# Kernel tuning notes

Hardware: AMD Instinct MI355X
Metric: run time of the kernel (lower is better)

The kernel has to match this reference:

```python
import jax, jax.numpy as jnp
import numpy as np

N = 100000      # total nodes across the batch of graphs
E = 1600000     # total edges (avg degree 16)
D = 128         # dim_drug (== num_feature here)
L = 3           # layer_drug
G = 2048        # number of graphs in the batch
BN_EPS = 1e-5


def setup_inputs() -> dict:
    key = jax.random.key(0)
    ks = jax.random.split(key, 10)
    x = jax.random.normal(ks[0], (N, D), dtype=jnp.float32)
    edge_index = jax.random.randint(ks[1], (2, E), 0, N, dtype=jnp.int64)
    batch = jnp.sort(jax.random.randint(ks[2], (N,), 0, G, dtype=jnp.int64))
    s = 0.05
    W1 = jax.random.normal(ks[3], (L, D, D), dtype=jnp.float32) * s
    b1 = jax.random.normal(ks[4], (L, D), dtype=jnp.float32) * s
    W2 = jax.random.normal(ks[5], (L, D, D), dtype=jnp.float32) * s
    b2 = jax.random.normal(ks[6], (L, D), dtype=jnp.float32) * s
    gamma = jnp.ones((L, D), dtype=jnp.float32)
    beta = jnp.zeros((L, D), dtype=jnp.float32)
    return {"x": x, "edge_index": edge_index, "batch": batch,
            "W1": W1, "b1": b1, "W2": W2, "b2": b2,
            "gamma": gamma, "beta": beta}


def reference(x, edge_index, batch, W1, b1, W2, b2, gamma, beta):
    src, dst = edge_index[0], edge_index[1]
    h = x
    layer_outs = []
    for i in range(L):
        # GINConv, eps=0: MLP( (1+eps)*h + sum_{j->i} h_j )
        agg = jax.ops.segment_sum(h[src], dst, num_segments=N)  # [N, D]
        m = agg + h
        m = jax.nn.relu(m @ W1[i] + b1[i]) @ W2[i] + b2[i]       # 2-layer MLP
        m = jax.nn.relu(m)                                        # F.relu after conv
        # BatchNorm1d (training mode: batch stats over node dim, biased var)
        mean = jnp.mean(m, axis=0)
        var = jnp.mean((m - mean) ** 2, axis=0)
        h = gamma[i] * (m - mean) * jax.lax.rsqrt(var + BN_EPS) + beta[i]
        layer_outs.append(h)
    node_rep = jnp.concatenate(layer_outs, axis=1)  # JK 'cat' -> [N, L*D]
    return jax.ops.segment_max(node_rep, batch, num_segments=G)  # [G, L*D]
```

## Files before the change

kernel.cpp:

```cpp
#include <hip/hip_runtime.h>
#include <stdint.h>

#define NN 100000
#define NE 1600000
#define DD 128
#define NL 3
#define NG 2048
#define BN_EPS 1e-5f
#define CAP 56
#define NXCD 8
#define WIN 12500

typedef short s16x8 __attribute__((ext_vector_type(8)));
typedef float f32x4 __attribute__((ext_vector_type(4)));

__device__ __forceinline__ unsigned short f2bfu(float f) {
    union { float f; unsigned int i; } x; x.f = f;
    unsigned int r = x.i + 0x7fffu + ((x.i >> 16) & 1u);
    return (unsigned short)(r >> 16);
}
__device__ __forceinline__ float bfu2f(unsigned short u) {
    union { unsigned int i; float f; } x; x.i = ((unsigned int)u) << 16; return x.f;
}
__device__ __forceinline__ float uplo(unsigned int u) {
    union { unsigned int i; float f; } x; x.i = u << 16; return x.f;
}
__device__ __forceinline__ float uphi(unsigned int u) {
    union { unsigned int i; float f; } x; x.i = u & 0xffff0000u; return x.f;
}
__device__ __forceinline__ void add8(float* a, uint4 v) {
    a[0] += uplo(v.x); a[1] += uphi(v.x);
    a[2] += uplo(v.y); a[3] += uphi(v.y);
    a[4] += uplo(v.z); a[5] += uphi(v.z);
    a[6] += uplo(v.w); a[7] += uphi(v.w);
}
__device__ __forceinline__ unsigned int pack2(float a, float b) {
    return (unsigned int)f2bfu(a) | ((unsigned int)f2bfu(b) << 16);
}

__global__ __launch_bounds__(256) void k_cvt(
    const float* __restrict__ x, unsigned short* __restrict__ hb)
{
    int i = (blockIdx.x * 256 + threadIdx.x) * 4;
    if (i >= NN * DD) return;
    float4 v = *(const float4*)(x + i);
    ushort4 o;
    o.x = f2bfu(v.x); o.y = f2bfu(v.y); o.z = f2bfu(v.z); o.w = f2bfu(v.w);
    *(ushort4*)(hb + i) = o;
}

__global__ __launch_bounds__(256) void k_wtrans(
    const float* __restrict__ W1, const float* __restrict__ W2,
    unsigned short* __restrict__ Wt)
{
    int idx = blockIdx.x * 256 + threadIdx.x;
    if (idx >= 6 * DD * DD) return;
    int mat = idx >> 14;
    int r = idx & 16383;
    int n = r >> 7, k = r & 127;
    const float* src = (mat < 3) ? (W1 + mat * DD * DD) : (W2 + (mat - 3) * DD * DD);
    Wt[idx] = f2bfu(src[k * DD + n]);
}

__global__ __launch_bounds__(256) void k_bounds(
    const int* __restrict__ batch, int* __restrict__ start)
{
    int n = blockIdx.x * 256 + threadIdx.x;
    if (n >= NN) return;
    int bn = batch[n];
    bn = bn < 0 ? 0 : (bn > NG - 1 ? NG - 1 : bn);
    int bp;
    if (n == 0) bp = -1;
    else {
        bp = batch[n - 1];
        bp = bp < 0 ? 0 : (bp > NG - 1 ? NG - 1 : bp);
    }
    for (int g = bp + 1; g <= bn; ++g) start[g] = n;
    if (n == NN - 1) {
        for (int g = bn + 1; g <= NG; ++g) start[g] = NN;
    }
}

__global__ __launch_bounds__(256) void k_fill2(
    const int* __restrict__ ei, int* __restrict__ cnt, int* __restrict__ csr)
{
    const int xcd = blockIdx.x & 7;
    const int slice = blockIdx.x >> 3;
    const int wlo = xcd * WIN, whi = wlo + WIN;
    int e0 = (slice * 256 + threadIdx.x) * 4;
    if (e0 >= NE) return;
    const int* dp = ei + NE + e0;
    int dd[4];
    dd[0] = __builtin_nontemporal_load(dp + 0);
    dd[1] = __builtin_nontemporal_load(dp + 1);
    dd[2] = __builtin_nontemporal_load(dp + 2);
    dd[3] = __builtin_nontemporal_load(dp + 3);
    bool any = false;
    #pragma unroll
    for (int i = 0; i < 4; ++i)
        any |= (dd[i] >= wlo && dd[i] < whi);
    if (!any) return;
    const int* sp = ei + e0;
    int ss[4];
    ss[0] = __builtin_nontemporal_load(sp + 0);
    ss[1] = __builtin_nontemporal_load(sp + 1);
    ss[2] = __builtin_nontemporal_load(sp + 2);
    ss[3] = __builtin_nontemporal_load(sp + 3);
    #pragma unroll
    for (int i = 0; i < 4; ++i) {
        int src = ss[i], dst = dd[i];
        if (dst < wlo || dst >= whi) continue;
        if ((unsigned)src >= NN) continue;
        int pos = atomicAdd(&cnt[dst], 1);
        if (pos < CAP) csr[dst * CAP + pos] = src;
    }
}

__global__ __launch_bounds__(256) void k_agg(
    const unsigned short* __restrict__ hb, const int* __restrict__ cnt,
    const int* __restrict__ csr, unsigned short* __restrict__ aggf)
{
    const int node = blockIdx.x * 16 + (threadIdx.x >> 4);
    const int lane = threadIdx.x & 15;
    if (node >= NN) return;
    int deg = cnt[node];
    deg = deg > CAP ? CAP : deg;
    const int* bkt = csr + node * CAP;
    const unsigned short* base = hb + lane * 8;
    float acc[8];
    {
        uint4 v = *(const uint4*)(base + (long long)node * DD);
        acc[0] = uplo(v.x); acc[1] = uphi(v.x);
        acc[2] = uplo(v.y); acc[3] = uphi(v.y);
        acc[4] = uplo(v.z); acc[5] = uphi(v.z);
        acc[6] = uplo(v.w); acc[7] = uphi(v.w);
    }
    int e = 0;
    for (; e + 8 <= deg; e += 8) {
        int4 i0 = *(const int4*)(bkt + e);
        int4 i1 = *(const int4*)(bkt + e + 4);
        uint4 v0 = *(const uint4*)(base + (long long)i0.x * DD);
        uint4 v1 = *(const uint4*)(base + (long long)i0.y * DD);
        uint4 v2 = *(const uint4*)(base + (long long)i0.z * DD);
        uint4 v3 = *(const uint4*)(base + (long long)i0.w * DD);
        uint4 v4 = *(const uint4*)(base + (long long)i1.x * DD);
        uint4 v5 = *(const uint4*)(base + (long long)i1.y * DD);
        uint4 v6 = *(const uint4*)(base + (long long)i1.z * DD);
        uint4 v7 = *(const uint4*)(base + (long long)i1.w * DD);
        add8(acc, v0); add8(acc, v1); add8(acc, v2); add8(acc, v3);
        add8(acc, v4); add8(acc, v5); add8(acc, v6); add8(acc, v7);
    }
    for (; e + 4 <= deg; e += 4) {
        int4 i0 = *(const int4*)(bkt + e);
        uint4 v0 = *(const uint4*)(base + (long long)i0.x * DD);
        uint4 v1 = *(const uint4*)(base + (long long)i0.y * DD);
        uint4 v2 = *(const uint4*)(base + (long long)i0.z * DD);
        uint4 v3 = *(const uint4*)(base + (long long)i0.w * DD);
        add8(acc, v0); add8(acc, v1); add8(acc, v2); add8(acc, v3);
    }
    for (; e < deg; ++e) {
        uint4 v = *(const uint4*)(base + (long long)bkt[e] * DD);
        add8(acc, v);
    }
    uint4 o;
    o.x = pack2(acc[0], acc[1]);
    o.y = pack2(acc[2], acc[3]);
    o.z = pack2(acc[4], acc[5]);
    o.w = pack2(acc[6], acc[7]);
    *(uint4*)(aggf + (long long)node * DD + lane * 8) = o;
}

__global__ __launch_bounds__(256, 2) void k_mlp(
    const unsigned short* __restrict__ aggf, unsigned short* __restrict__ hb,
    const unsigned short* __restrict__ W1t, const float* __restrict__ b1,
    const unsigned short* __restrict__ W2t, const float* __restrict__ b2,
    float* __restrict__ stats)
{
    __shared__ unsigned short lA[128 * 136];
    __shared__ unsigned short lW[128 * 136];
    __shared__ float sSum[4][128];
    __shared__ float sSq[4][128];
    const int tid = threadIdx.x;
    const int row0 = blockIdx.x * 128;

    #pragma unroll
    for (int it = 0; it < 8; ++it) {
        int eidx = (it * 256 + tid) * 8;
        int r = eidx >> 7, c = eidx & 127;
        *(uint4*)(&lW[r * 136 + c]) = *(const uint4*)(W1t + eidx);
    }
    {
        int col8 = tid & 15, rr = tid >> 4;
        #pragma unroll
        for (int it = 0; it < 8; ++it) {
            int r = rr + it * 16;
            int grow = row0 + r;
            uint4 v;
            if (grow < NN) {
                v = *(const uint4*)(aggf + (long long)grow * DD + col8 * 8);
            } else {
                v.x = v.y = v.z = v.w = 0;
            }
            *(uint4*)(&lA[r * 136 + col8 * 8]) = v;
        }
    }
    __syncthreads();

    const int wave = tid >> 6, lane = tid & 63;
    const int quad = lane >> 4, m16 = lane & 15;

    f32x4 acc[2][8] = {};
    #pragma unroll
    for (int k0 = 0; k0 < 128; k0 += 32) {
        const int kk = k0 + quad * 8;
        s16x8 a0 = *(const s16x8*)(&lA[(wave * 32 + m16) * 136 + kk]);
        s16x8 a1 = *(const s16x8*)(&lA[(wave * 32 + 16 + m16) * 136 + kk]);
        #pragma unroll
        for (int ct = 0; ct < 8; ++ct) {
            s16x8 bf = *(const s16x8*)(&lW[(ct * 16 + m16) * 136 + kk]);
            acc[0][ct] = __builtin_amdgcn_mfma_f32_16x16x32_bf16(a0, bf, acc[0][ct], 0, 0, 0);
            acc[1][ct] = __builtin_amdgcn_mfma_f32_16x16x32_bf16(a1, bf, acc[1][ct], 0, 0, 0);
        }
    }
    __syncthreads();

    #pragma unroll
    for (int rt = 0; rt < 2; ++rt) {
        #pragma unroll
        for (int ct = 0; ct < 8; ++ct) {
            int col = ct * 16 + m16;
            float b = b1[col];
            #pragma unroll
            for (int r = 0; r < 4; ++r) {
                int lrow = wave * 32 + rt * 16 + quad * 4 + r;
                lA[lrow * 136 + col] = f2bfu(fmaxf(acc[rt][ct][r] + b, 0.0f));
            }
        }
    }
    #pragma unroll
    for (int it = 0; it < 8; ++it) {
        int eidx = (it * 256 + tid) * 8;
        int r = eidx >> 7, c = eidx & 127;
        *(uint4*)(&lW[r * 136 + c]) = *(const uint4*)(W2t + eidx);
    }
    __syncthreads();

    #pragma unroll
    for (int rt = 0; rt < 2; ++rt)
        #pragma unroll
        for (int ct = 0; ct < 8; ++ct)
            acc[rt][ct] = f32x4{0.f, 0.f, 0.f, 0.f};
    #pragma unroll
    for (int k0 = 0; k0 < 128; k0 += 32) {
        const int kk = k0 + quad * 8;
        s16x8 a0 = *(const s16x8*)(&lA[(wave * 32 + m16) * 136 + kk]);
        s16x8 a1 = *(const s16x8*)(&lA[(wave * 32 + 16 + m16) * 136 + kk]);
        #pragma unroll
        for (int ct = 0; ct < 8; ++ct) {
            s16x8 bf = *(const s16x8*)(&lW[(ct * 16 + m16) * 136 + kk]);
            acc[0][ct] = __builtin_amdgcn_mfma_f32_16x16x32_bf16(a0, bf, acc[0][ct], 0, 0, 0);
            acc[1][ct] = __builtin_amdgcn_mfma_f32_16x16x32_bf16(a1, bf, acc[1][ct], 0, 0, 0);
        }
    }

    float csum[8] = {}, csq[8] = {};
    #pragma unroll
    for (int rt = 0; rt < 2; ++rt) {
        int rbase = row0 + wave * 32 + rt * 16 + quad * 4;
        #pragma unroll
        for (int ct = 0; ct < 8; ++ct) {
            int col = ct * 16 + m16;
            float b = b2[col];
            #pragma unroll
            for (int r = 0; r < 4; ++r) {
                int row = rbase + r;
                if (row < NN) {
                    float v = fmaxf(acc[rt][ct][r] + b, 0.0f);
                    hb[(long long)row * DD + col] = f2bfu(v);
                    csum[ct] += v;
                    csq[ct] += v * v;
                }
            }
        }
    }
    #pragma unroll
    for (int ct = 0; ct < 8; ++ct) {
        csum[ct] += __shfl_xor(csum[ct], 16);
        csum[ct] += __shfl_xor(csum[ct], 32);
        csq[ct]  += __shfl_xor(csq[ct], 16);
        csq[ct]  += __shfl_xor(csq[ct], 32);
    }
    if (quad == 0) {
        #pragma unroll
        for (int ct = 0; ct < 8; ++ct) {
            int col = ct * 16 + m16;
            sSum[wave][col] = csum[ct];
            sSq[wave][col] = csq[ct];
        }
    }
    __syncthreads();
    if (tid < 128) {
        float s = sSum[0][tid] + sSum[1][tid] + sSum[2][tid] + sSum[3][tid];
        float q = sSq[0][tid] + sSq[1][tid] + sSq[2][tid] + sSq[3][tid];
        atomicAdd(&stats[tid], s);
        atomicAdd(&stats[DD + tid], q);
    }
}

template <bool WR>
__global__ __launch_bounds__(256) void k_norm(
    unsigned short* __restrict__ hb, const float* __restrict__ stats,
    const float* __restrict__ gamma, const float* __restrict__ beta,
    const int* __restrict__ start, float* __restrict__ out, int layer)
{
    __shared__ float sMx[256];
    const int d = threadIdx.x & 127;
    const int half = threadIdx.x >> 7;
    const int g = blockIdx.x;
    const float inv_n = 1.0f / (float)NN;
    float mean = stats[d] * inv_n;
    float var = stats[DD + d] * inv_n - mean * mean;
    float inv = rsqrtf(fmaxf(var, 0.f) + BN_EPS);
    float a = gamma[d] * inv;
    float c = beta[d] - mean * a;
    int n0 = start[g], n1 = start[g + 1];
    n0 = n0 < 0 ? 0 : (n0 > NN ? NN : n0);
    n1 = n1 < 0 ? 0 : (n1 > NN ? NN : n1);
    float mx = -3.0e38f;
    for (int n = n0 + half; n < n1; n += 2) {
        float v = bfu2f(hb[(long long)n * DD + d]);
        float hv = a * v + c;
        if (WR) hb[(long long)n * DD + d] = f2bfu(hv);
        mx = fmaxf(mx, hv);
    }
    sMx[threadIdx.x] = mx;
    __syncthreads();
    if (threadIdx.x < 128) {
        float m = fmaxf(sMx[d], sMx[d + 128]);
        if (n1 <= n0) m = 0.f;
        out[(long long)g * (NL * DD) + layer * DD + d] = m;
    }
}

extern "C" void kernel_launch(void* const* d_in, const int* in_sizes, int n_in,
                              void* d_out, int out_size, void* d_ws, size_t ws_size,
                              hipStream_t stream) {
    const float* x     = (const float*)d_in[0];
    const int*   ei    = (const int*)d_in[1];
    const int*   batch = (const int*)d_in[2];
    const float* W1    = (const float*)d_in[3];
    const float* b1    = (const float*)d_in[4];
    const float* W2    = (const float*)d_in[5];
    const float* b2    = (const float*)d_in[6];
    const float* gamma = (const float*)d_in[7];
    const float* beta  = (const float*)d_in[8];
    float* out = (float*)d_out;
    unsigned short* aggf = (unsigned short*)d_in[0];

    char* p = (char*)d_ws;
    float*          stats = (float*)p;
    int*            cnt   = (int*)(p + 4096);
    int*            start = (int*)(p + 405504);
    unsigned short* Wt    = (unsigned short*)(p + 417792);
    int*            csr   = (int*)(p + 614400);
    unsigned short* hb    = (unsigned short*)(p + 23014400);

    hipMemsetAsync(p, 0, 404096, stream);
    k_cvt<<<(NN * DD / 4 + 255) / 256, 256, 0, stream>>>(x, hb);
    k_wtrans<<<(6 * DD * DD + 255) / 256, 256, 0, stream>>>(W1, W2, Wt);
    k_bounds<<<(NN + 255) / 256, 256, 0, stream>>>(batch, start);
    {
        int slices = (NE / 4 + 255) / 256;
        k_fill2<<<slices * NXCD, 256, 0, stream>>>(ei, cnt, csr);
    }

    for (int l = 0; l < NL; ++l) {
        float* stats_l = stats + l * 256;
        k_agg<<<(NN + 15) / 16, 256, 0, stream>>>(hb, cnt, csr, aggf);
        k_mlp<<<(NN + 127) / 128, 256, 0, stream>>>(aggf, hb,
                                                    Wt + l * DD * DD, b1 + l * DD,
                                                    Wt + (3 + l) * DD * DD, b2 + l * DD,
                                                    stats_l);
        if (l < NL - 1)
            k_norm<true><<<NG, 256, 0, stream>>>(hb, stats_l, gamma + l * DD,
                                                 beta + l * DD, start, out, l);
        else
            k_norm<false><<<NG, 256, 0, stream>>>(hb, stats_l, gamma + l * DD,
                                                  beta + l * DD, start, out, l);
    }
}
```

Measured before the change: 539.3 us.

## Bin edges by destination window before per-XCD CSR fill

Replaces the CSR build, in which each of the eight XCD-window passes re-read the whole edge list, with two stages. A binning kernel reads every edge once and writes packed (local dst, src) words into eight per-window bins using LDS counters and one global atomic per block. A fill kernel then reads only its own window's bin. This cuts repeated edge-list reads, at the cost of an extra pass and bins stored in the x input buffer, which is overwritten before k_cvt finishes reading it? Bins are written after k_cvt, so the order is fine, but edges past the fixed BINCAP per window are silently dropped.

```diff
diff --git a/kernel.cpp b/kernel.cpp
--- a/kernel.cpp
+++ b/kernel.cpp
@@ -10,6 +10,7 @@
 #define CAP 56
 #define NXCD 8
 #define WIN 12500
+#define BINCAP 208896
 
 typedef short s16x8 __attribute__((ext_vector_type(8)));
 typedef float f32x4 __attribute__((ext_vector_type(4)));
@@ -81,38 +82,89 @@
     }
 }
 
-__global__ __launch_bounds__(256) void k_fill2(
-    const int* __restrict__ ei, int* __restrict__ cnt, int* __restrict__ csr)
-{
-    const int xcd = blockIdx.x & 7;
+__global__ __launch_bounds__(256) void k_bin(
+    const int* __restrict__ ei, int* __restrict__ bincnt,
+    unsigned int* __restrict__ bins)
+{
+    __shared__ int lcnt[NXCD];
+    __shared__ int lbase[NXCD];
+    const int tid = threadIdx.x;
+    if (tid < NXCD) lcnt[tid] = 0;
+    __syncthreads();
+
+    int e0 = (blockIdx.x * 256 + tid) * 4;
+    int w[4], lp[4];
+    unsigned int pk[4];
+    bool vld[4] = {false, false, false, false};
+    if (e0 < NE) {
+        const int* dp = ei + NE + e0;
+        const int* sp = ei + e0;
+        int dd[4], ss[4];
+        dd[0] = __builtin_nontemporal_load(dp + 0);
+        dd[1] = __builtin_nontemporal_load(dp + 1);
+        dd[2] = __builtin_nontemporal_load(dp + 2);
+        dd[3] = __builtin_nontemporal_load(dp + 3);
+        ss[0] = __builtin_nontemporal_load(sp + 0);
+        ss[1] = __builtin_nontemporal_load(sp + 1);
+        ss[2] = __builtin_nontemporal_load(sp + 2);
+        ss[3] = __builtin_nontemporal_load(sp + 3);
+        #pragma unroll
+        for (int i = 0; i < 4; ++i) {
+            int dst = dd[i], src = ss[i];
+            if ((unsigned)dst < NN && (unsigned)src < NN) {
+                int wi = dst / WIN;
+                w[i] = wi;
+                pk[i] = ((unsigned)(dst - wi * WIN) << 17) | (unsigned)src;
+                lp[i] = atomicAdd(&lcnt[wi], 1);
+                vld[i] = true;
+            }
+        }
+    }
+    __syncthreads();
+    if (tid < NXCD) lbase[tid] = atomicAdd(&bincnt[tid], lcnt[tid]);
+    __syncthreads();
+    #pragma unroll
+    for (int i = 0; i < 4; ++i) {
+        if (vld[i]) {
+            int idx = lbase[w[i]] + lp[i];
+            if (idx < BINCAP)
+                bins[(long long)w[i] * BINCAP + idx] = pk[i];
+        }
+    }
+}
+
+__global__ __launch_bounds__(256) void k_fillb(
+    const int* __restrict__ bincnt, const unsigned int* __restrict__ bins,
+    int* __restrict__ cnt, int* __restrict__ csr)
+{
+    const int w = blockIdx.x & 7;
     const int slice = blockIdx.x >> 3;
-    const int wlo = xcd * WIN, whi = wlo + WIN;
+    int count = bincnt[w];
+    count = count > BINCAP ? BINCAP : count;
     int e0 = (slice * 256 + threadIdx.x) * 4;
-    if (e0 >= NE) return;
-    const int* dp = ei + NE + e0;
-    int dd[4];
-    dd[0] = __builtin_nontemporal_load(dp + 0);
-    dd[1] = __builtin_nontemporal_load(dp + 1);
-    dd[2] = __builtin_nontemporal_load(dp + 2);
-    dd[3] = __builtin_nontemporal_load(dp + 3);
-    bool any = false;
-    #pragma unroll
-    for (int i = 0; i < 4; ++i)
-        any |= (dd[i] >= wlo && dd[i] < whi);
-    if (!any) return;
-    const int* sp = ei + e0;
-    int ss[4];
-    ss[0] = __builtin_nontemporal_load(sp + 0);
-    ss[1] = __builtin_nontemporal_load(sp + 1);
-    ss[2] = __builtin_nontemporal_load(sp + 2);
-    ss[3] = __builtin_nontemporal_load(sp + 3);
+    if (e0 >= count) return;
+    const unsigned int* bp = bins + (long long)w * BINCAP + e0;
+    const int wlo = w * WIN;
+    unsigned int u[4];
+    int nv = count - e0;
+    if (nv >= 4) {
+        uint4 q;
+        q.x = __builtin_nontemporal_load(bp + 0);
+        q.y = __builtin_nontemporal_load(bp + 1);
+        q.z = __builtin_nontemporal_load(bp + 2);
+        q.w = __builtin_nontemporal_load(bp + 3);
+        u[0] = q.x; u[1] = q.y; u[2] = q.z; u[3] = q.w;
+        nv = 4;
+    } else {
+        for (int i = 0; i < nv; ++i) u[i] = bp[i];
+    }
     #pragma unroll
     for (int i = 0; i < 4; ++i) {
-        int src = ss[i], dst = dd[i];
-        if (dst < wlo || dst >= whi) continue;
-        if ((unsigned)src >= NN) continue;
-        int pos = atomicAdd(&cnt[dst], 1);
-        if (pos < CAP) csr[dst * CAP + pos] = src;
+        if (i >= nv) break;
+        int src = (int)(u[i] & 0x1FFFFu);
+        int node = wlo + (int)(u[i] >> 17);
+        int pos = atomicAdd(&cnt[node], 1);
+        if (pos < CAP) csr[node * CAP + pos] = src;
     }
 }
 
@@ -356,23 +408,23 @@
     const float* beta  = (const float*)d_in[8];
     float* out = (float*)d_out;
     unsigned short* aggf = (unsigned short*)d_in[0];
+    unsigned int*   bins = (unsigned int*)d_in[0];
 
     char* p = (char*)d_ws;
-    float*          stats = (float*)p;
-    int*            cnt   = (int*)(p + 4096);
-    int*            start = (int*)(p + 405504);
-    unsigned short* Wt    = (unsigned short*)(p + 417792);
-    int*            csr   = (int*)(p + 614400);
-    unsigned short* hb    = (unsigned short*)(p + 23014400);
+    float*          stats  = (float*)p;
+    int*            bincnt = (int*)(p + 3072);
+    int*            cnt    = (int*)(p + 4096);
+    int*            start  = (int*)(p + 405504);
+    unsigned short* Wt     = (unsigned short*)(p + 417792);
+    int*            csr    = (int*)(p + 614400);
+    unsigned short* hb     = (unsigned short*)(p + 23014400);
 
     hipMemsetAsync(p, 0, 404096, stream);
     k_cvt<<<(NN * DD / 4 + 255) / 256, 256, 0, stream>>>(x, hb);
     k_wtrans<<<(6 * DD * DD + 255) / 256, 256, 0, stream>>>(W1, W2, Wt);
     k_bounds<<<(NN + 255) / 256, 256, 0, stream>>>(batch, start);
-    {
-        int slices = (NE / 4 + 255) / 256;
-        k_fill2<<<slices * NXCD, 256, 0, stream>>>(ei, cnt, csr);
-    }
+    k_bin<<<(NE / 4 + 255) / 256, 256, 0, stream>>>(ei, bincnt, bins);
+    k_fillb<<<(BINCAP / 1024) * NXCD, 256, 0, stream>>>(bincnt, bins, cnt, csr);
 
     for (int l = 0; l < NL; ++l) {
         float* stats_l = stats + l * 256;
```

Result: slower. 557.0 us (+3.3%).
